# Kernel optimization log

Measured on AMD Instinct MI355X. Metric: run time of the kernel, lower is better.

## Reference

```python
import jax, jax.numpy as jnp
import numpy as np

LN_EPS = 1e-5


def _layernorm_hd(x, gamma, beta):
    # normalize jointly over the last two dims (H, D), matching nn.LayerNorm((H, D))
    m = jnp.mean(x, axis=(-2, -1), keepdims=True)
    v = jnp.var(x, axis=(-2, -1), keepdims=True)
    return (x - m) * jax.lax.rsqrt(v + LN_EPS) * gamma + beta


def setup_inputs() -> dict:
    B, S, H, D = 4, 4096, 8, 64
    key = jax.random.key(0)
    k1, k2, k3 = jax.random.split(key, 3)
    heads_input = jax.random.normal(k1, (B, S, H, D), dtype=jnp.float32)
    W_hid = jax.random.normal(k2, (2 * D, 3 * D), dtype=jnp.float32) * (1.0 / np.sqrt(2 * D))
    b_hid = jnp.zeros((3 * D,), dtype=jnp.float32)
    W_og = jax.random.normal(k3, (2 * D, D), dtype=jnp.float32) * (1.0 / np.sqrt(2 * D))
    b_og = jnp.zeros((D,), dtype=jnp.float32)
    ln_gamma = jnp.ones((H, D), dtype=jnp.float32)
    ln_beta = jnp.zeros((H, D), dtype=jnp.float32)
    init_cx = jnp.zeros((H, D), dtype=jnp.float32)
    return {"heads_input": heads_input, "W_hid": W_hid, "b_hid": b_hid,
            "W_og": W_og, "b_og": b_og, "ln_gamma": ln_gamma,
            "ln_beta": ln_beta, "init_cx": init_cx}


def reference(heads_input, W_hid, b_hid, W_og, b_og, ln_gamma, ln_beta, init_cx):
    B, S, H, D = heads_input.shape
    # RS1cumsumFunc: exclusive (right-shifted) cumsum along seq of detached input
    x_det = jax.lax.stop_gradient(heads_input)
    cs = jnp.cumsum(x_det, axis=1)
    csum_raw = jnp.concatenate([jnp.zeros_like(cs[:, :1]), cs[:, :-1]], axis=1)
    csum = _layernorm_hd(csum_raw, ln_gamma, ln_beta)

    # trans_hid on concat(heads_input, csum): [B,S,H,2D] -> [B,S,H,3D]
    hid_in = jnp.concatenate([heads_input, csum], axis=-1)
    h3 = jnp.einsum('bshd,de->bshe', hid_in, W_hid) + b_hid
    igate, fgate, hidden = jnp.split(h3, 3, axis=-1)
    fg = jax.nn.sigmoid(fgate)
    igh = jax.nn.sigmoid(igate) * jax.nn.relu(hidden)

    # LGateFunc: cell_t = fg_t * cell_{t-1} + igh_t, cell_{-1} = init_cx
    def combine(c1, c2):
        a1, b1 = c1
        a2, b2 = c2
        return a1 * a2, b1 * a2 + b2

    a, b = jax.lax.associative_scan(combine, (fg, igh), axis=1)
    cell = a * init_cx + b  # init_cx [H,D] broadcasts over [B,S,H,D]

    og_in = jnp.concatenate([heads_input, cell], axis=-1)
    og = jax.nn.sigmoid(jnp.einsum('bshd,de->bshe', og_in, W_og) + b_og)
    return og * cell
```

## Files before the change

### kernel.cpp

```cpp
#include <hip/hip_runtime.h>
#include <math.h>

#define S_   4096
#define H_   8
#define D_   64
#define HD_  512
#define NCH  256
#define LCH  16
#define RC   128

typedef __bf16 bf16x8 __attribute__((ext_vector_type(8)));
typedef float  f32x4  __attribute__((ext_vector_type(4)));

__device__ __forceinline__ float sigm(float v) { return 1.f / (1.f + __expf(-v)); }

__global__ __launch_bounds__(256) void k_wt(const float* __restrict__ Wh,
                                            const float* __restrict__ Wo,
                                            __bf16* __restrict__ Wth,
                                            __bf16* __restrict__ Wto) {
  int idx = blockIdx.x * 256 + threadIdx.x;
  if (idx < 24576) {
    int k = idx / 192, n = idx % 192;
    Wth[n * 128 + k] = (__bf16)Wh[idx];
  } else {
    int j = idx - 24576;
    int k = j >> 6, n = j & 63;
    Wto[n * 128 + k] = (__bf16)Wo[j];
  }
}

__global__ __launch_bounds__(512) void k_chunk_sums(const float* __restrict__ x,
                                                    float* __restrict__ sums) {
  const int b = blockIdx.x >> 8, c = blockIdx.x & 255;
  const int t = threadIdx.x;
  const float* p = x + ((size_t)b * S_ + c * LCH) * HD_ + t;
  float acc = 0.f;
  #pragma unroll
  for (int i = 0; i < LCH; ++i) acc += p[(size_t)i * HD_];
  sums[((size_t)b * NCH + c) * HD_ + t] = acc;
}

__global__ __launch_bounds__(512) void k_scan_offsets(float* __restrict__ sums) {
  const int b = blockIdx.x, t = threadIdx.x;
  float run = 0.f;
  for (int c0 = 0; c0 < NCH; c0 += 8) {
    float v[8];
    #pragma unroll
    for (int i = 0; i < 8; ++i)
      v[i] = sums[((size_t)b * NCH + c0 + i) * HD_ + t];
    #pragma unroll
    for (int i = 0; i < 8; ++i) {
      sums[((size_t)b * NCH + c0 + i) * HD_ + t] = run;
      run += v[i];
    }
  }
}

__global__ __launch_bounds__(512) void k_ln(const float* __restrict__ x,
                                            const float* __restrict__ offs,
                                            const float* __restrict__ gamma,
                                            const float* __restrict__ beta,
                                            __bf16* __restrict__ Abf) {
  __shared__ float2 red[2][8];
  const int b = blockIdx.x >> 8, c = blockIdx.x & 255;
  const int t = threadIdx.x;
  float run = offs[((size_t)b * NCH + c) * HD_ + t];
  const float g = gamma[t], be = beta[t];
  const size_t xbase = ((size_t)b * S_ + c * LCH) * HD_ + t;
  const int h = t >> 6, d = t & 63;
  const size_t rbase = ((size_t)b * NCH + c) * 128 + h * 16;
  float xv = x[xbase];
  for (int i = 0; i < LCH; ++i) {
    float xn = (i < LCH - 1) ? x[xbase + (size_t)(i + 1) * HD_] : 0.f;
    float v = run, v2 = run * run;
    #pragma unroll
    for (int o = 32; o; o >>= 1) { v += __shfl_xor(v, o); v2 += __shfl_xor(v2, o); }
    if ((t & 63) == 0) red[i & 1][t >> 6] = make_float2(v, v2);
    __syncthreads();
    float s1 = 0.f, s2 = 0.f;
    #pragma unroll
    for (int w = 0; w < 8; ++w) { s1 += red[i & 1][w].x; s2 += red[i & 1][w].y; }
    float m = s1 * (1.f / HD_);
    float var = fmaf(-m, m, s2 * (1.f / HD_));
    float inv = rsqrtf(var + 1e-5f);
    size_t r = rbase + i;
    Abf[r * 128 + 64 + d] = (__bf16)((run - m) * inv * g + be);
    Abf[r * 128 + d] = (__bf16)xv;
    run += xv;
    xv = xn;
  }
}

__global__ __launch_bounds__(256) void k_gates(const __bf16* __restrict__ Abf,
                                               const __bf16* __restrict__ Wt,
                                               const float* __restrict__ bh,
                                               float* __restrict__ ga,
                                               float* __restrict__ gb,
                                               float* __restrict__ cA,
                                               float* __restrict__ cB) {
  const int t = threadIdx.x;
  const int wave = t >> 6, lane = t & 63;
  const int quad = lane >> 4, l16 = lane & 15;
  const int r0 = blockIdx.x * RC;

  f32x4 acc[2][12];
  #pragma unroll
  for (int i = 0; i < 2; ++i)
    #pragma unroll
    for (int j = 0; j < 12; ++j) acc[i][j] = (f32x4){0.f, 0.f, 0.f, 0.f};

  #pragma unroll
  for (int ks = 0; ks < 4; ++ks) {
    bf16x8 bfrag[12];
    #pragma unroll
    for (int nt = 0; nt < 12; ++nt)
      bfrag[nt] = *(const bf16x8*)(Wt + (nt * 16 + l16) * 128 + ks * 32 + quad * 8);
    #pragma unroll
    for (int mi = 0; mi < 2; ++mi) {
      int mt = wave * 2 + mi;
      bf16x8 afrag = *(const bf16x8*)(Abf + (size_t)(r0 + mt * 16 + l16) * 128 + ks * 32 + quad * 8);
      #pragma unroll
      for (int nt = 0; nt < 12; ++nt)
        acc[mi][nt] = __builtin_amdgcn_mfma_f32_16x16x32_bf16(afrag, bfrag[nt], acc[mi][nt], 0, 0, 0);
    }
  }

  #pragma unroll
  for (int mi = 0; mi < 2; ++mi) {
    int mt = wave * 2 + mi;
    #pragma unroll
    for (int nt = 0; nt < 4; ++nt) {
      int dcol = nt * 16 + l16;
      float bi = bh[dcol], bf_ = bh[64 + dcol], bhv = bh[128 + dcol];
      float pa[4], pb[4];
      float a = 1.f, bb = 0.f;
      #pragma unroll
      for (int r = 0; r < 4; ++r) {
        float ip = acc[mi][nt][r] + bi;
        float fp = acc[mi][nt + 4][r] + bf_;
        float hp = acc[mi][nt + 8][r] + bhv;
        float fv = sigm(fp);
        float gv = sigm(ip) * fmaxf(hp, 0.f);
        a = fv * a;
        bb = fmaf(fv, bb, gv);
        pa[r] = a; pb[r] = bb;
      }
      float exA = 1.f, exB = 0.f;
      #pragma unroll
      for (int q = 0; q < 3; ++q) {
        float Aq = __shfl(a, q * 16 + l16, 64);
        float Bq = __shfl(bb, q * 16 + l16, 64);
        if (q < quad) { exB = fmaf(Aq, exB, Bq); exA = Aq * exA; }
      }
      float ra3 = 0.f, rb3 = 0.f;
      #pragma unroll
      for (int r = 0; r < 4; ++r) {
        float ra = pa[r] * exA;
        float rb = fmaf(pa[r], exB, pb[r]);
        size_t row = (size_t)(r0 + mt * 16 + quad * 4 + r);
        ga[row * 64 + dcol] = ra;
        gb[row * 64 + dcol] = rb;
        ra3 = ra; rb3 = rb;
      }
      if (quad == 3) {
        cA[(size_t)blockIdx.x * 512 + mt * 64 + dcol] = ra3;
        cB[(size_t)blockIdx.x * 512 + mt * 64 + dcol] = rb3;
      }
    }
  }
}

__global__ __launch_bounds__(512) void k_cell_scan(float* __restrict__ cA,
                                                   const float* __restrict__ cB,
                                                   const float* __restrict__ initcx) {
  const int b = blockIdx.x, t = threadIdx.x;
  float run = initcx[t];
  for (int c0 = 0; c0 < NCH; c0 += 8) {
    float av[8], bv[8];
    #pragma unroll
    for (int i = 0; i < 8; ++i) {
      size_t idx = ((size_t)b * NCH + c0 + i) * HD_ + t;
      av[i] = cA[idx];
      bv[i] = cB[idx];
    }
    #pragma unroll
    for (int i = 0; i < 8; ++i) {
      size_t idx = ((size_t)b * NCH + c0 + i) * HD_ + t;
      cA[idx] = run;
      run = fmaf(av[i], run, bv[i]);
    }
  }
}

__global__ __launch_bounds__(256) void k_og(const __bf16* __restrict__ Abf,
                                            const float* __restrict__ ga,
                                            const float* __restrict__ gb,
                                            const float* __restrict__ cin,
                                            const __bf16* __restrict__ Wt,
                                            const float* __restrict__ bo,
                                            float* __restrict__ out) {
  __shared__ float cl[RC * 68];
  const int t = threadIdx.x;
  const int wave = t >> 6, lane = t & 63;
  const int quad = lane >> 4, l16 = lane & 15;
  const int r0 = blockIdx.x * RC;
  const int b4 = blockIdx.x >> 8, c = blockIdx.x & 255;

  #pragma unroll
  for (int mi = 0; mi < 2; ++mi) {
    int mt = wave * 2 + mi;
    #pragma unroll
    for (int nt = 0; nt < 4; ++nt) {
      int dcol = nt * 16 + l16;
      float ci = cin[(size_t)blockIdx.x * 512 + mt * 64 + dcol];
      #pragma unroll
      for (int r = 0; r < 4; ++r) {
        int rowl = mt * 16 + quad * 4 + r;
        size_t row = (size_t)(r0 + rowl);
        float cv = fmaf(ga[row * 64 + dcol], ci, gb[row * 64 + dcol]);
        cl[rowl * 68 + dcol] = cv;
      }
    }
  }
  __syncthreads();

  f32x4 acc[2][4];
  #pragma unroll
  for (int i = 0; i < 2; ++i)
    #pragma unroll
    for (int j = 0; j < 4; ++j) acc[i][j] = (f32x4){0.f, 0.f, 0.f, 0.f};

  #pragma unroll
  for (int ks = 0; ks < 4; ++ks) {
    bf16x8 bfrag[4];
    #pragma unroll
    for (int nt = 0; nt < 4; ++nt)
      bfrag[nt] = *(const bf16x8*)(Wt + (nt * 16 + l16) * 128 + ks * 32 + quad * 8);
    #pragma unroll
    for (int mi = 0; mi < 2; ++mi) {
      int mt = wave * 2 + mi;
      bf16x8 afrag;
      if (ks < 2) {
        afrag = *(const bf16x8*)(Abf + (size_t)(r0 + mt * 16 + l16) * 128 + ks * 32 + quad * 8);
      } else {
        int rowl = mt * 16 + l16;
        const float* src = &cl[rowl * 68 + (ks - 2) * 32 + quad * 8];
        #pragma unroll
        for (int j = 0; j < 8; ++j) afrag[j] = (__bf16)src[j];
      }
      #pragma unroll
      for (int nt = 0; nt < 4; ++nt)
        acc[mi][nt] = __builtin_amdgcn_mfma_f32_16x16x32_bf16(afrag, bfrag[nt], acc[mi][nt], 0, 0, 0);
    }
  }

  #pragma unroll
  for (int mi = 0; mi < 2; ++mi) {
    int mt = wave * 2 + mi;
    #pragma unroll
    for (int nt = 0; nt < 4; ++nt) {
      int dcol = nt * 16 + l16;
      float bv = bo[dcol];
      #pragma unroll
      for (int r = 0; r < 4; ++r) {
        int rowl = mt * 16 + quad * 4 + r;
        int s = quad * 4 + r;
        float og = sigm(acc[mi][nt][r] + bv);
        out[(((size_t)b4 * S_ + c * LCH + s) * H_ + mt) * 64 + dcol] = og * cl[rowl * 68 + dcol];
      }
    }
  }
}

extern "C" void kernel_launch(void* const* d_in, const int* in_sizes, int n_in,
                              void* d_out, int out_size, void* d_ws, size_t ws_size,
                              hipStream_t stream) {
  const float* x      = (const float*)d_in[0];
  const float* W_hid  = (const float*)d_in[1];
  const float* b_hid  = (const float*)d_in[2];
  const float* W_og   = (const float*)d_in[3];
  const float* b_og   = (const float*)d_in[4];
  const float* gamma  = (const float*)d_in[5];
  const float* beta   = (const float*)d_in[6];
  const float* initcx = (const float*)d_in[7];
  float* out = (float*)d_out;
  float* ws  = (float*)d_ws;

  float*  buf0 = ws;
  float*  buf1 = ws + 524288;
  __bf16* Abf  = (__bf16*)(ws + 1048576);
  float*  ga   = ws + 1048576 + 8388608;
  float*  gb   = ga + 8388608;
  __bf16* Wth  = (__bf16*)(gb + 8388608);
  __bf16* Wto  = Wth + 24576;

  k_wt          <<<128,  256, 0, stream>>>(W_hid, W_og, Wth, Wto);
  k_chunk_sums  <<<1024, 512, 0, stream>>>(x, buf0);
  k_scan_offsets<<<4,    512, 0, stream>>>(buf0);
  k_ln          <<<1024, 512, 0, stream>>>(x, buf0, gamma, beta, Abf);
  k_gates       <<<1024, 256, 0, stream>>>(Abf, Wth, b_hid, ga, gb, buf0, buf1);
  k_cell_scan   <<<4,    512, 0, stream>>>(buf0, buf1, initcx);
  k_og          <<<1024, 256, 0, stream>>>(Abf, ga, gb, buf0, Wto, b_og, out);
}
```

Measured before the change: 223.1 us.

## Fuse layernorm into gate GEMM, recompute gates in output pass, hierarchical scans

Fuses the cumsum layernorm into the gate GEMM kernel, with the bf16 activation tile kept in swizzled shared memory instead of a global buffer. The output kernel recomputes layernorm and gates rather than reading stored per-row ga/gb arrays, so only chunk totals go to global memory. The two serial 4-block scans (prefix offsets and cell carry) become three-level parallel scans. This removes large intermediate global traffic and the low-parallelism scan kernels, at the cost of doing the layernorm and gate GEMM work twice and adding more kernel launches.

Result: slower. 255.6 us (+14.5%).

```diff
diff --git a/kernel.cpp b/kernel.cpp
--- a/kernel.cpp
+++ b/kernel.cpp
@@ -8,11 +8,17 @@
 #define NCH  256
 #define LCH  16
 #define RC   128
+#define NCOL 2048
 
 typedef __bf16 bf16x8 __attribute__((ext_vector_type(8)));
+typedef __bf16 bf16x2 __attribute__((ext_vector_type(2)));
 typedef float  f32x4  __attribute__((ext_vector_type(4)));
 
 __device__ __forceinline__ float sigm(float v) { return 1.f / (1.f + __expf(-v)); }
+
+__device__ __forceinline__ int swzA(int row, int bytecol) {
+  return row * 256 + (bytecol ^ ((row & 7) << 4));
+}
 
 __global__ __launch_bounds__(256) void k_wt(const float* __restrict__ Wh,
                                             const float* __restrict__ Wo,
@@ -40,233 +46,328 @@
   sums[((size_t)b * NCH + c) * HD_ + t] = acc;
 }
 
-__global__ __launch_bounds__(512) void k_scan_offsets(float* __restrict__ sums) {
-  const int b = blockIdx.x, t = threadIdx.x;
+__global__ __launch_bounds__(256) void kx_l1(const float* __restrict__ sums,
+                                             float* __restrict__ gx) {
+  int w = blockIdx.x * 256 + threadIdx.x;
+  int grp = w >> 11, col = w & 2047;
+  int b = col >> 9, hd = col & 511;
+  float s = 0.f;
+  #pragma unroll
+  for (int i = 0; i < 16; ++i)
+    s += sums[((size_t)(b * NCH + grp * 16 + i)) * HD_ + hd];
+  gx[grp * NCOL + col] = s;
+}
+__global__ __launch_bounds__(256) void kx_l2(float* __restrict__ gx) {
+  int col = blockIdx.x * 256 + threadIdx.x;
   float run = 0.f;
-  for (int c0 = 0; c0 < NCH; c0 += 8) {
-    float v[8];
-    #pragma unroll
-    for (int i = 0; i < 8; ++i)
-      v[i] = sums[((size_t)b * NCH + c0 + i) * HD_ + t];
-    #pragma unroll
-    for (int i = 0; i < 8; ++i) {
-      sums[((size_t)b * NCH + c0 + i) * HD_ + t] = run;
-      run += v[i];
-    }
-  }
-}
-
-__global__ __launch_bounds__(512) void k_ln(const float* __restrict__ x,
-                                            const float* __restrict__ offs,
-                                            const float* __restrict__ gamma,
-                                            const float* __restrict__ beta,
-                                            __bf16* __restrict__ Abf) {
-  __shared__ float2 red[2][8];
-  const int b = blockIdx.x >> 8, c = blockIdx.x & 255;
-  const int t = threadIdx.x;
-  float run = offs[((size_t)b * NCH + c) * HD_ + t];
-  const float g = gamma[t], be = beta[t];
-  const size_t xbase = ((size_t)b * S_ + c * LCH) * HD_ + t;
-  const int h = t >> 6, d = t & 63;
-  const size_t rbase = ((size_t)b * NCH + c) * 128 + h * 16;
-  float xv = x[xbase];
-  for (int i = 0; i < LCH; ++i) {
-    float xn = (i < LCH - 1) ? x[xbase + (size_t)(i + 1) * HD_] : 0.f;
-    float v = run, v2 = run * run;
-    #pragma unroll
-    for (int o = 32; o; o >>= 1) { v += __shfl_xor(v, o); v2 += __shfl_xor(v2, o); }
-    if ((t & 63) == 0) red[i & 1][t >> 6] = make_float2(v, v2);
-    __syncthreads();
-    float s1 = 0.f, s2 = 0.f;
-    #pragma unroll
-    for (int w = 0; w < 8; ++w) { s1 += red[i & 1][w].x; s2 += red[i & 1][w].y; }
-    float m = s1 * (1.f / HD_);
-    float var = fmaf(-m, m, s2 * (1.f / HD_));
-    float inv = rsqrtf(var + 1e-5f);
-    size_t r = rbase + i;
-    Abf[r * 128 + 64 + d] = (__bf16)((run - m) * inv * g + be);
-    Abf[r * 128 + d] = (__bf16)xv;
-    run += xv;
-    xv = xn;
-  }
-}
-
-__global__ __launch_bounds__(256) void k_gates(const __bf16* __restrict__ Abf,
-                                               const __bf16* __restrict__ Wt,
-                                               const float* __restrict__ bh,
-                                               float* __restrict__ ga,
-                                               float* __restrict__ gb,
-                                               float* __restrict__ cA,
-                                               float* __restrict__ cB) {
+  #pragma unroll
+  for (int g = 0; g < 16; ++g) {
+    float v = gx[g * NCOL + col];
+    gx[g * NCOL + col] = run;
+    run += v;
+  }
+}
+__global__ __launch_bounds__(256) void kx_l3(float* __restrict__ sums,
+                                             const float* __restrict__ gx) {
+  int w = blockIdx.x * 256 + threadIdx.x;
+  int grp = w >> 11, col = w & 2047;
+  int b = col >> 9, hd = col & 511;
+  float run = gx[grp * NCOL + col];
+  #pragma unroll
+  for (int i = 0; i < 16; ++i) {
+    size_t idx = ((size_t)(b * NCH + grp * 16 + i)) * HD_ + hd;
+    float v = sums[idx];
+    sums[idx] = run;
+    run += v;
+  }
+}
+
+template <bool WRITE_TOT>
+__device__ __forceinline__ void ln_gates(const float* __restrict__ x,
+                                         const float* __restrict__ offs,
+                                         const float* __restrict__ gamma,
+                                         const float* __restrict__ beta,
+                                         const __bf16* __restrict__ Wth,
+                                         const float* __restrict__ bh,
+                                         char* Al, float2* red,
+                                         int b, int c, int cid,
+                                         float (&abA)[2][16], float (&abB)[2][16],
+                                         float* __restrict__ cA,
+                                         float* __restrict__ cB) {
   const int t = threadIdx.x;
   const int wave = t >> 6, lane = t & 63;
   const int quad = lane >> 4, l16 = lane & 15;
-  const int r0 = blockIdx.x * RC;
-
-  f32x4 acc[2][12];
-  #pragma unroll
-  for (int i = 0; i < 2; ++i)
-    #pragma unroll
-    for (int j = 0; j < 12; ++j) acc[i][j] = (f32x4){0.f, 0.f, 0.f, 0.f};
-
-  #pragma unroll
-  for (int ks = 0; ks < 4; ++ks) {
-    bf16x8 bfrag[12];
-    #pragma unroll
-    for (int nt = 0; nt < 12; ++nt)
-      bfrag[nt] = *(const bf16x8*)(Wt + (nt * 16 + l16) * 128 + ks * 32 + quad * 8);
-    #pragma unroll
-    for (int mi = 0; mi < 2; ++mi) {
-      int mt = wave * 2 + mi;
-      bf16x8 afrag = *(const bf16x8*)(Abf + (size_t)(r0 + mt * 16 + l16) * 128 + ks * 32 + quad * 8);
-      #pragma unroll
-      for (int nt = 0; nt < 12; ++nt)
-        acc[mi][nt] = __builtin_amdgcn_mfma_f32_16x16x32_bf16(afrag, bfrag[nt], acc[mi][nt], 0, 0, 0);
-    }
-  }
+
+  {
+    const int hd0 = 2 * t;
+    const int h = hd0 >> 6, d0 = hd0 & 63;
+    float2 rr = *(const float2*)(offs + (size_t)(b * NCH + c) * HD_ + hd0);
+    float run0 = rr.x, run1 = rr.y;
+    float2 gg = *(const float2*)(gamma + hd0);
+    float2 be = *(const float2*)(beta + hd0);
+    const size_t xbase = ((size_t)b * S_ + c * LCH) * HD_;
+    float2 xv = *(const float2*)(x + xbase + hd0);
+    for (int s = 0; s < LCH; ++s) {
+      float2 xn = make_float2(0.f, 0.f);
+      if (s < LCH - 1) xn = *(const float2*)(x + xbase + (size_t)(s + 1) * HD_ + hd0);
+      float v = run0 + run1;
+      float v2 = fmaf(run0, run0, run1 * run1);
+      #pragma unroll
+      for (int o = 32; o; o >>= 1) { v += __shfl_xor(v, o); v2 += __shfl_xor(v2, o); }
+      if (lane == 0) red[(s & 1) * 4 + wave] = make_float2(v, v2);
+      __syncthreads();
+      const float2* rb = red + (s & 1) * 4;
+      float s1 = rb[0].x + rb[1].x + rb[2].x + rb[3].x;
+      float s2 = rb[0].y + rb[1].y + rb[2].y + rb[3].y;
+      float m = s1 * (1.f / HD_);
+      float var = fmaf(-m, m, s2 * (1.f / HD_));
+      float inv = rsqrtf(var + 1e-5f);
+      int row = h * 16 + s;
+      bf16x2 px = { (__bf16)xv.x, (__bf16)xv.y };
+      bf16x2 pl = { (__bf16)((run0 - m) * inv * gg.x + be.x),
+                    (__bf16)((run1 - m) * inv * gg.y + be.y) };
+      *(bf16x2*)(Al + swzA(row, d0 * 2)) = px;
+      *(bf16x2*)(Al + swzA(row, 128 + d0 * 2)) = pl;
+      run0 += xv.x; run1 += xv.y;
+      xv = xn;
+    }
+  }
+  __syncthreads();
 
   #pragma unroll
   for (int mi = 0; mi < 2; ++mi) {
-    int mt = wave * 2 + mi;
+    const int mt = wave * 2 + mi;
+    const int arow = mt * 16 + l16;
+    float fv[16], iv[16];
+    {
+      f32x4 acc[4];
+      #pragma unroll
+      for (int nt = 0; nt < 4; ++nt) acc[nt] = (f32x4){0.f, 0.f, 0.f, 0.f};
+      #pragma unroll
+      for (int ks = 0; ks < 4; ++ks) {
+        bf16x8 af = *(const bf16x8*)(Al + swzA(arow, ks * 64 + quad * 16));
+        #pragma unroll
+        for (int nt = 0; nt < 4; ++nt) {
+          bf16x8 bf_ = *(const bf16x8*)(Wth + ((4 + nt) * 16 + l16) * 128 + ks * 32 + quad * 8);
+          acc[nt] = __builtin_amdgcn_mfma_f32_16x16x32_bf16(af, bf_, acc[nt], 0, 0, 0);
+        }
+      }
+      #pragma unroll
+      for (int nt = 0; nt < 4; ++nt) {
+        float bb_ = bh[64 + nt * 16 + l16];
+        #pragma unroll
+        for (int r = 0; r < 4; ++r) fv[nt * 4 + r] = sigm(acc[nt][r] + bb_);
+      }
+    }
+    {
+      f32x4 acc[4];
+      #pragma unroll
+      for (int nt = 0; nt < 4; ++nt) acc[nt] = (f32x4){0.f, 0.f, 0.f, 0.f};
+      #pragma unroll
+      for (int ks = 0; ks < 4; ++ks) {
+        bf16x8 af = *(const bf16x8*)(Al + swzA(arow, ks * 64 + quad * 16));
+        #pragma unroll
+        for (int nt = 0; nt < 4; ++nt) {
+          bf16x8 bf_ = *(const bf16x8*)(Wth + (nt * 16 + l16) * 128 + ks * 32 + quad * 8);
+          acc[nt] = __builtin_amdgcn_mfma_f32_16x16x32_bf16(af, bf_, acc[nt], 0, 0, 0);
+        }
+      }
+      #pragma unroll
+      for (int nt = 0; nt < 4; ++nt) {
+        float bb_ = bh[nt * 16 + l16];
+        #pragma unroll
+        for (int r = 0; r < 4; ++r) iv[nt * 4 + r] = sigm(acc[nt][r] + bb_);
+      }
+    }
+    {
+      f32x4 acc[4];
+      #pragma unroll
+      for (int nt = 0; nt < 4; ++nt) acc[nt] = (f32x4){0.f, 0.f, 0.f, 0.f};
+      #pragma unroll
+      for (int ks = 0; ks < 4; ++ks) {
+        bf16x8 af = *(const bf16x8*)(Al + swzA(arow, ks * 64 + quad * 16));
+        #pragma unroll
+        for (int nt = 0; nt < 4; ++nt) {
+          bf16x8 bf_ = *(const bf16x8*)(Wth + ((8 + nt) * 16 + l16) * 128 + ks * 32 + quad * 8);
+          acc[nt] = __builtin_amdgcn_mfma_f32_16x16x32_bf16(af, bf_, acc[nt], 0, 0, 0);
+        }
+      }
+      #pragma unroll
+      for (int nt = 0; nt < 4; ++nt) {
+        float bb_ = bh[128 + nt * 16 + l16];
+        #pragma unroll
+        for (int r = 0; r < 4; ++r)
+          iv[nt * 4 + r] = iv[nt * 4 + r] * fmaxf(acc[nt][r] + bb_, 0.f);
+      }
+    }
     #pragma unroll
     for (int nt = 0; nt < 4; ++nt) {
-      int dcol = nt * 16 + l16;
-      float bi = bh[dcol], bf_ = bh[64 + dcol], bhv = bh[128 + dcol];
-      float pa[4], pb[4];
-      float a = 1.f, bb = 0.f;
+      float a = 1.f, bb2 = 0.f, pa[4], pb[4];
       #pragma unroll
       for (int r = 0; r < 4; ++r) {
-        float ip = acc[mi][nt][r] + bi;
-        float fp = acc[mi][nt + 4][r] + bf_;
-        float hp = acc[mi][nt + 8][r] + bhv;
-        float fv = sigm(fp);
-        float gv = sigm(ip) * fmaxf(hp, 0.f);
-        a = fv * a;
-        bb = fmaf(fv, bb, gv);
-        pa[r] = a; pb[r] = bb;
-      }
-      float exA = 1.f, exB = 0.f;
-      #pragma unroll
-      for (int q = 0; q < 3; ++q) {
-        float Aq = __shfl(a, q * 16 + l16, 64);
-        float Bq = __shfl(bb, q * 16 + l16, 64);
-        if (q < quad) { exB = fmaf(Aq, exB, Bq); exA = Aq * exA; }
-      }
-      float ra3 = 0.f, rb3 = 0.f;
-      #pragma unroll
-      for (int r = 0; r < 4; ++r) {
-        float ra = pa[r] * exA;
-        float rb = fmaf(pa[r], exB, pb[r]);
-        size_t row = (size_t)(r0 + mt * 16 + quad * 4 + r);
-        ga[row * 64 + dcol] = ra;
-        gb[row * 64 + dcol] = rb;
-        ra3 = ra; rb3 = rb;
-      }
-      if (quad == 3) {
-        cA[(size_t)blockIdx.x * 512 + mt * 64 + dcol] = ra3;
-        cB[(size_t)blockIdx.x * 512 + mt * 64 + dcol] = rb3;
-      }
-    }
-  }
-}
-
-__global__ __launch_bounds__(512) void k_cell_scan(float* __restrict__ cA,
-                                                   const float* __restrict__ cB,
-                                                   const float* __restrict__ initcx) {
-  const int b = blockIdx.x, t = threadIdx.x;
-  float run = initcx[t];
-  for (int c0 = 0; c0 < NCH; c0 += 8) {
-    float av[8], bv[8];
-    #pragma unroll
-    for (int i = 0; i < 8; ++i) {
-      size_t idx = ((size_t)b * NCH + c0 + i) * HD_ + t;
-      av[i] = cA[idx];
-      bv[i] = cB[idx];
-    }
-    #pragma unroll
-    for (int i = 0; i < 8; ++i) {
-      size_t idx = ((size_t)b * NCH + c0 + i) * HD_ + t;
-      cA[idx] = run;
-      run = fmaf(av[i], run, bv[i]);
-    }
-  }
-}
-
-__global__ __launch_bounds__(256) void k_og(const __bf16* __restrict__ Abf,
-                                            const float* __restrict__ ga,
-                                            const float* __restrict__ gb,
-                                            const float* __restrict__ cin,
-                                            const __bf16* __restrict__ Wt,
-                                            const float* __restrict__ bo,
-                                            float* __restrict__ out) {
-  __shared__ float cl[RC * 68];
+        float fvv = fv[nt * 4 + r], gvv = iv[nt * 4 + r];
+        a = fvv * a;
+        bb2 = fmaf(fvv, bb2, gvv);
+        pa[r] = a; pb[r] = bb2;
+      }
+      if constexpr (WRITE_TOT) {
+        float TA = 1.f, TB = 0.f;
+        #pragma unroll
+        for (int q = 0; q < 4; ++q) {
+          float Aq = __shfl(a, q * 16 + l16, 64);
+          float Bq = __shfl(bb2, q * 16 + l16, 64);
+          TB = fmaf(Aq, TB, Bq);
+          TA = Aq * TA;
+        }
+        if (quad == 0) {
+          cA[(size_t)cid * HD_ + mt * 64 + nt * 16 + l16] = TA;
+          cB[(size_t)cid * HD_ + mt * 64 + nt * 16 + l16] = TB;
+        }
+      } else {
+        float exA = 1.f, exB = 0.f;
+        #pragma unroll
+        for (int q = 0; q < 3; ++q) {
+          float Aq = __shfl(a, q * 16 + l16, 64);
+          float Bq = __shfl(bb2, q * 16 + l16, 64);
+          if (q < quad) { exB = fmaf(Aq, exB, Bq); exA = Aq * exA; }
+        }
+        #pragma unroll
+        for (int r = 0; r < 4; ++r) {
+          abA[mi][nt * 4 + r] = pa[r] * exA;
+          abB[mi][nt * 4 + r] = fmaf(pa[r], exB, pb[r]);
+        }
+      }
+    }
+  }
+}
+
+__global__ __launch_bounds__(256, 4) void k_gates_f(const float* __restrict__ x,
+                                                    const float* __restrict__ offs,
+                                                    const float* __restrict__ gamma,
+                                                    const float* __restrict__ beta,
+                                                    const __bf16* __restrict__ Wth,
+                                                    const float* __restrict__ bh,
+                                                    float* __restrict__ cA,
+                                                    float* __restrict__ cB) {
+  __shared__ char Al[RC * 256];
+  __shared__ float2 red[8];
+  const int cid = blockIdx.x, b = cid >> 8, c = cid & 255;
+  float abA[2][16], abB[2][16];
+  ln_gates<true>(x, offs, gamma, beta, Wth, bh, Al, red, b, c, cid, abA, abB, cA, cB);
+}
+
+__global__ __launch_bounds__(256) void kc_l1(const float* __restrict__ cA,
+                                             const float* __restrict__ cB,
+                                             float* __restrict__ gA,
+                                             float* __restrict__ gB) {
+  int w = blockIdx.x * 256 + threadIdx.x;
+  int grp = w >> 11, col = w & 2047;
+  int b = col >> 9, hd = col & 511;
+  float Ag = 1.f, Bg = 0.f;
+  #pragma unroll
+  for (int i = 0; i < 16; ++i) {
+    size_t idx = ((size_t)(b * NCH + grp * 16 + i)) * HD_ + hd;
+    float Ac = cA[idx], Bc = cB[idx];
+    Bg = fmaf(Ac, Bg, Bc);
+    Ag = Ac * Ag;
+  }
+  gA[grp * NCOL + col] = Ag;
+  gB[grp * NCOL + col] = Bg;
+}
+__global__ __launch_bounds__(256) void kc_l2(float* __restrict__ gA,
+                                             const float* __restrict__ gB,
+                                             const float* __restrict__ initcx) {
+  int col = blockIdx.x * 256 + threadIdx.x;
+  int hd = col & 511;
+  float run = initcx[hd];
+  #pragma unroll
+  for (int g = 0; g < 16; ++g) {
+    float Ag = gA[g * NCOL + col], Bg = gB[g * NCOL + col];
+    gA[g * NCOL + col] = run;
+    run = fmaf(Ag, run, Bg);
+  }
+}
+__global__ __launch_bounds__(256) void kc_l3(const float* __restrict__ cA,
+                                             const float* __restrict__ cB,
+                                             const float* __restrict__ gA,
+                                             float* __restrict__ cin) {
+  int w = blockIdx.x * 256 + threadIdx.x;
+  int grp = w >> 11, col = w & 2047;
+  int b = col >> 9, hd = col & 511;
+  float run = gA[grp * NCOL + col];
+  #pragma unroll
+  for (int i = 0; i < 16; ++i) {
+    size_t idx = ((size_t)(b * NCH + grp * 16 + i)) * HD_ + hd;
+    cin[idx] = run;
+    run = fmaf(cA[idx], run, cB[idx]);
+  }
+}
+
+__global__ __launch_bounds__(256, 4) void k_og_f(const float* __restrict__ x,
+                                                 const float* __restrict__ offs,
+                                                 const float* __restrict__ gamma,
+                                                 const float* __restrict__ beta,
+                                                 const __bf16* __restrict__ Wth,
+                                                 const __bf16* __restrict__ Wto,
+                                                 const float* __restrict__ bh,
+                                                 const float* __restrict__ bo,
+                                                 const float* __restrict__ cin,
+                                                 float* __restrict__ out) {
+  __shared__ char Al[RC * 256];
+  __shared__ float2 red[8];
+  const int cid = blockIdx.x, b = cid >> 8, c = cid & 255;
   const int t = threadIdx.x;
   const int wave = t >> 6, lane = t & 63;
   const int quad = lane >> 4, l16 = lane & 15;
-  const int r0 = blockIdx.x * RC;
-  const int b4 = blockIdx.x >> 8, c = blockIdx.x & 255;
-
+
+  float abA[2][16], abB[2][16];
+  ln_gates<false>(x, offs, gamma, beta, Wth, bh, Al, red, b, c, cid,
+                  abA, abB, nullptr, nullptr);
+
+  float cell[2][16];
   #pragma unroll
   for (int mi = 0; mi < 2; ++mi) {
-    int mt = wave * 2 + mi;
+    const int mt = wave * 2 + mi;
     #pragma unroll
     for (int nt = 0; nt < 4; ++nt) {
-      int dcol = nt * 16 + l16;
-      float ci = cin[(size_t)blockIdx.x * 512 + mt * 64 + dcol];
+      const int dcol = nt * 16 + l16;
+      float ci = cin[(size_t)cid * HD_ + mt * 64 + dcol];
       #pragma unroll
       for (int r = 0; r < 4; ++r) {
         int rowl = mt * 16 + quad * 4 + r;
-        size_t row = (size_t)(r0 + rowl);
-        float cv = fmaf(ga[row * 64 + dcol], ci, gb[row * 64 + dcol]);
-        cl[rowl * 68 + dcol] = cv;
+        float cv = fmaf(abA[mi][nt * 4 + r], ci, abB[mi][nt * 4 + r]);
+        cell[mi][nt * 4 + r] = cv;
+        *(__bf16*)(Al + swzA(rowl, 128 + dcol * 2)) = (__bf16)cv;
       }
     }
   }
   __syncthreads();
 
-  f32x4 acc[2][4];
-  #pragma unroll
-  for (int i = 0; i < 2; ++i)
+  #pragma unroll
+  for (int mi = 0; mi < 2; ++mi) {
+    const int mt = wave * 2 + mi;
+    const int arow = mt * 16 + l16;
+    f32x4 acc[4];
     #pragma unroll
-    for (int j = 0; j < 4; ++j) acc[i][j] = (f32x4){0.f, 0.f, 0.f, 0.f};
-
-  #pragma unroll
-  for (int ks = 0; ks < 4; ++ks) {
-    bf16x8 bfrag[4];
+    for (int nt = 0; nt < 4; ++nt) acc[nt] = (f32x4){0.f, 0.f, 0.f, 0.f};
     #pragma unroll
-    for (int nt = 0; nt < 4; ++nt)
-      bfrag[nt] = *(const bf16x8*)(Wt + (nt * 16 + l16) * 128 + ks * 32 + quad * 8);
-    #pragma unroll
-    for (int mi = 0; mi < 2; ++mi) {
-      int mt = wave * 2 + mi;
-      bf16x8 afrag;
-      if (ks < 2) {
-        afrag = *(const bf16x8*)(Abf + (size_t)(r0 + mt * 16 + l16) * 128 + ks * 32 + quad * 8);
-      } else {
-        int rowl = mt * 16 + l16;
-        const float* src = &cl[rowl * 68 + (ks - 2) * 32 + quad * 8];
-        #pragma unroll
-        for (int j = 0; j < 8; ++j) afrag[j] = (__bf16)src[j];
-      }
-      #pragma unroll
-      for (int nt = 0; nt < 4; ++nt)
-        acc[mi][nt] = __builtin_amdgcn_mfma_f32_16x16x32_bf16(afrag, bfrag[nt], acc[mi][nt], 0, 0, 0);
-    }
-  }
-
-  #pragma unroll
-  for (int mi = 0; mi < 2; ++mi) {
-    int mt = wave * 2 + mi;
+    for (int ks = 0; ks < 4; ++ks) {
+      bf16x8 af = *(const bf16x8*)(Al + swzA(arow, ks * 64 + quad * 16));
+      #pragma unroll
+      for (int nt = 0; nt < 4; ++nt) {
+        bf16x8 bf_ = *(const bf16x8*)(Wto + (nt * 16 + l16) * 128 + ks * 32 + quad * 8);
+        acc[nt] = __builtin_amdgcn_mfma_f32_16x16x32_bf16(af, bf_, acc[nt], 0, 0, 0);
+      }
+    }
     #pragma unroll
     for (int nt = 0; nt < 4; ++nt) {
-      int dcol = nt * 16 + l16;
+      const int dcol = nt * 16 + l16;
       float bv = bo[dcol];
       #pragma unroll
       for (int r = 0; r < 4; ++r) {
-        int rowl = mt * 16 + quad * 4 + r;
         int s = quad * 4 + r;
-        float og = sigm(acc[mi][nt][r] + bv);
-        out[(((size_t)b4 * S_ + c * LCH + s) * H_ + mt) * 64 + dcol] = og * cl[rowl * 68 + dcol];
+        float og = sigm(acc[nt][r] + bv);
+        out[(((size_t)b * S_ + c * LCH + s) * H_ + mt) * D_ + dcol] = og * cell[mi][nt * 4 + r];
       }
     }
   }
@@ -287,18 +388,24 @@
   float* ws  = (float*)d_ws;
 
   float*  buf0 = ws;
-  float*  buf1 = ws + 524288;
-  __bf16* Abf  = (__bf16*)(ws + 1048576);
-  float*  ga   = ws + 1048576 + 8388608;
-  float*  gb   = ga + 8388608;
-  __bf16* Wth  = (__bf16*)(gb + 8388608);
+  float*  cA   = ws + 524288;
+  float*  cB   = cA + 524288;
+  float*  cin  = cB + 524288;
+  float*  gx   = cin + 524288;
+  float*  gA   = gx + 32768;
+  float*  gB   = gA + 32768;
+  __bf16* Wth  = (__bf16*)(gB + 32768);
   __bf16* Wto  = Wth + 24576;
 
-  k_wt          <<<128,  256, 0, stream>>>(W_hid, W_og, Wth, Wto);
-  k_chunk_sums  <<<1024, 512, 0, stream>>>(x, buf0);
-  k_scan_offsets<<<4,    512, 0, stream>>>(buf0);
-  k_ln          <<<1024, 512, 0, stream>>>(x, buf0, gamma, beta, Abf);
-  k_gates       <<<1024, 256, 0, stream>>>(Abf, Wth, b_hid, ga, gb, buf0, buf1);
-  k_cell_scan   <<<4,    512, 0, stream>>>(buf0, buf1, initcx);
-  k_og          <<<1024, 256, 0, stream>>>(Abf, ga, gb, buf0, Wto, b_og, out);
-}
+  k_wt         <<<128,  256, 0, stream>>>(W_hid, W_og, Wth, Wto);
+  k_chunk_sums <<<1024, 512, 0, stream>>>(x, buf0);
+  kx_l1        <<<128,  256, 0, stream>>>(buf0, gx);
+  kx_l2        <<<8,    256, 0, stream>>>(gx);
+  kx_l3        <<<128,  256, 0, stream>>>(buf0, gx);
+  k_gates_f    <<<1024, 256, 0, stream>>>(x, buf0, gamma, beta, Wth, b_hid, cA, cB);
+  kc_l1        <<<128,  256, 0, stream>>>(cA, cB, gA, gB);
+  kc_l2        <<<8,    256, 0, stream>>>(gA, gB, initcx);
+  kc_l3        <<<128,  256, 0, stream>>>(cA, cB, gA, cin);
+  k_og_f       <<<1024, 256, 0, stream>>>(x, buf0, gamma, beta, Wth, Wto,
+                                          b_hid, b_og, cin, out);
+}
```
